# Kernel optimization log

Hardware: AMD Instinct MI355X
Metric: run time of the kernel (lower is better)

The kernel has to match this reference:

```python
import jax, jax.numpy as jnp
import numpy as np

B, H, S, D = 2, 8, 2048, 64

def setup_inputs() -> dict:
    key = jax.random.key(0)
    ks = jax.random.split(key, 6)
    names = ["Qx", "Kx", "Vx", "Qy", "Ky", "Vy"]
    return {n: jax.random.normal(k, (B, H, S, D), dtype=jnp.float32)
            for n, k in zip(names, ks)}

def reference(Qx, Kx, Vx, Qy, Ky, Vy):
    scale = float(np.sqrt(Qx.shape[-1]))
    # Two score matmuls: [B,H,S,S] each
    ax = jnp.einsum('bhqd,bhkd->bhqk', Qx, Kx)
    ay = jnp.einsum('bhqd,bhkd->bhqk', Qy, Ky)
    # cat(dim=1) -> reshape(B,2,H,S,S) -> mean(dim=1) == elementwise average
    attn = (ax + ay) * 0.5
    # numerically stable softmax over keys; dropout is identity in eval mode
    w = jax.nn.softmax(attn / scale, axis=-1)
    # Shared attention weights into two value matmuls
    out1 = jnp.einsum('bhqk,bhkd->bhqd', w, Vx)
    out2 = jnp.einsum('bhqk,bhkd->bhqd', w, Vy)
    return (out1, out2)
```

## Files before the change

kernel.cpp:

```cpp
#include <hip/hip_runtime.h>
#include <hip/hip_bf16.h>

typedef __attribute__((ext_vector_type(4)))  float f32x4;
typedef __attribute__((ext_vector_type(16))) float f32x16;
typedef __attribute__((ext_vector_type(8)))  short s16x8;
typedef __attribute__((ext_vector_type(4)))  short s16x4;
typedef __attribute__((ext_vector_type(4)))  int   i32x4;

#define BB 2
#define HH 8
#define SS 2048
#define DD 64
#define QBLK 64
#define KBLK 64
#define NT   (SS / KBLK)
#define NBH  (BB * HH)

#define WS_KX 0
#define WS_KY ((size_t)NBH * NT * 8192)
#define WS_VX ((size_t)2 * NBH * NT * 8192)
#define WS_VY ((size_t)3 * NBH * NT * 8192)
#define WS_NEED ((size_t)4 * NBH * NT * 8192)

__device__ __forceinline__ short f2bf(float x) {
    unsigned u = __builtin_bit_cast(unsigned, x);
    u = (u + 0x7FFFu + ((u >> 16) & 1u)) >> 16;
    return (short)u;
}

__device__ __forceinline__ unsigned cvtpk(float lo, float hi) {
    unsigned d;
    asm("v_cvt_pk_bf16_f32 %0, %1, %2" : "=v"(d) : "v"(lo), "v"(hi));
    return d;
}

__device__ __forceinline__ int swz(int row, int byteInRow) {
    return row * 128 + (byteInRow ^ ((row & 7) << 4));
}

__device__ __forceinline__ void glds16(const void* g, void* l) {
    __builtin_amdgcn_global_load_lds(
        (const __attribute__((address_space(1))) unsigned*)g,
        (__attribute__((address_space(3))) unsigned*)l, 16, 0, 0);
}

__global__ __launch_bounds__(256)
void prep_kv(const float* __restrict__ Kx, const float* __restrict__ Ky,
             const float* __restrict__ Vx, const float* __restrict__ Vy,
             char* __restrict__ ws)
{
    const int b = blockIdx.x;
    if (b < 1024) {
        const int tid  = b * 256 + threadIdx.x;
        const int dblk = tid & 7;
        const int s    = (tid >> 3) & 2047;
        const int bh   = tid >> 14;
        const size_t gi = ((size_t)bh * SS + s) * DD + dblk * 8;
        const int kt = s >> 6, row = s & 63;
        const size_t dst = (size_t)(bh * NT + kt) * 8192 + swz(row, dblk * 16);
        const float* px = Kx + gi;
        const float* py = Ky + gi;
        s16x8 a, bb;
#pragma unroll
        for (int i = 0; i < 8; ++i) { a[i] = f2bf(px[i]); bb[i] = f2bf(py[i]); }
        *(s16x8*)(ws + WS_KX + dst) = a;
        *(s16x8*)(ws + WS_KY + dst) = bb;
    } else {
        const int tid  = (b - 1024) * 256 + threadIdx.x;
        const int d    = tid & 63;
        const int sblk = (tid >> 6) & 7;
        const int kt   = (tid >> 9) & 31;
        const int bh   = tid >> 14;
        const size_t gbase = ((size_t)bh * SS + kt * 64 + sblk * 8) * DD + d;
        s16x8 a, bb;
#pragma unroll
        for (int i = 0; i < 8; ++i) {
            a[i]  = f2bf(Vx[gbase + (size_t)i * DD]);
            bb[i] = f2bf(Vy[gbase + (size_t)i * DD]);
        }
        const size_t dst = (size_t)(bh * NT + kt) * 8192 + swz(d, sblk * 16);
        *(s16x8*)(ws + WS_VX + dst) = a;
        *(s16x8*)(ws + WS_VY + dst) = bb;
    }
}

__global__ __launch_bounds__(256, 2)
void attn_main(const float* __restrict__ Qx, const float* __restrict__ Qy,
               const char* __restrict__ ws, float* __restrict__ Out)
{
    extern __shared__ char lds[];

    const int t    = threadIdx.x;
    const int lane = t & 63;
    const int w    = t >> 6;
    const int qsub = w & 1;
    const int ks   = w >> 1;
    const int l31  = lane & 31;
    const int hi   = lane >> 5;

    int bid = blockIdx.x;
    bid = (bid & 7) * 64 + (bid >> 3);
    const int bh = bid >> 5;
    const int q0 = (bid & 31) * QBLK;
    const size_t base = (size_t)bh * SS * DD;

    const int qrow = q0 + qsub * 32 + l31;
    s16x8 qbx[4], qby[4];
#pragma unroll
    for (int dc = 0; dc < 4; ++dc) {
        const int d0 = dc * 16 + hi * 8;
        const float* qp = Qx + base + (size_t)qrow * DD + d0;
        const float* qq = Qy + base + (size_t)qrow * DD + d0;
        const float4 f0 = *(const float4*)qp;
        const float4 f1 = *(const float4*)(qp + 4);
        const float4 h0 = *(const float4*)qq;
        const float4 h1 = *(const float4*)(qq + 4);
        qbx[dc][0]=f2bf(f0.x); qbx[dc][1]=f2bf(f0.y); qbx[dc][2]=f2bf(f0.z); qbx[dc][3]=f2bf(f0.w);
        qbx[dc][4]=f2bf(f1.x); qbx[dc][5]=f2bf(f1.y); qbx[dc][6]=f2bf(f1.z); qbx[dc][7]=f2bf(f1.w);
        qby[dc][0]=f2bf(h0.x); qby[dc][1]=f2bf(h0.y); qby[dc][2]=f2bf(h0.z); qby[dc][3]=f2bf(h0.w);
        qby[dc][4]=f2bf(h1.x); qby[dc][5]=f2bf(h1.y); qby[dc][6]=f2bf(h1.z); qby[dc][7]=f2bf(h1.w);
    }

    f32x16 o1_0, o1_1, o2_0, o2_1;
#pragma unroll
    for (int j = 0; j < 16; ++j) { o1_0[j] = 0.f; o1_1[j] = 0.f; o2_0[j] = 0.f; o2_1[j] = 0.f; }
    float lsum = 0.f;

    const float SCL = 0.09016844005556021f;

#define STAGE(kt_, b_)                                                             \
    do {                                                                           \
        const size_t img_ = (size_t)(bh * NT + (kt_)) * 8192 + (size_t)t * 16;     \
        char* dst_ = lds + (b_) * 32768 + t * 16;                                  \
        glds16(ws + WS_KX + img_,        dst_);                                    \
        glds16(ws + WS_KX + img_ + 4096, dst_ + 4096);                             \
        glds16(ws + WS_KY + img_,        dst_ + 8192);                             \
        glds16(ws + WS_KY + img_ + 4096, dst_ + 12288);                            \
        glds16(ws + WS_VX + img_,        dst_ + 16384);                            \
        glds16(ws + WS_VX + img_ + 4096, dst_ + 20480);                            \
        glds16(ws + WS_VY + img_,        dst_ + 24576);                            \
        glds16(ws + WS_VY + img_ + 4096, dst_ + 28672);                            \
    } while (0)

#define QK_BLOCK(KxL_, KyL_, sc_)                                                  \
    do {                                                                           \
        _Pragma("unroll")                                                          \
        for (int dc = 0; dc < 4; ++dc) {                                           \
            const int off = swz(ks * 32 + l31, dc * 32 + hi * 16);                 \
            const s16x8 ka = *(const s16x8*)((KxL_) + off);                        \
            const s16x8 kb = *(const s16x8*)((KyL_) + off);                        \
            sc_ = __builtin_amdgcn_mfma_f32_32x32x16_bf16(ka, qbx[dc], sc_, 0, 0, 0); \
            sc_ = __builtin_amdgcn_mfma_f32_32x32x16_bf16(kb, qby[dc], sc_, 0, 0, 0); \
        }                                                                          \
    } while (0)

#define V_READS(VxL_, VyL_, vr_)                                                   \
    do {                                                                           \
        _Pragma("unroll")                                                          \
        for (int ch = 0; ch < 2; ++ch) {                                           \
            const int off0 = swz(l31,      ks * 64 + ch * 32 + hi * 16);           \
            const int off1 = swz(32 + l31, ks * 64 + ch * 32 + hi * 16);           \
            vr_[ch * 4 + 0] = *(const s16x8*)((VxL_) + off0);                      \
            vr_[ch * 4 + 1] = *(const s16x8*)((VxL_) + off1);                      \
            vr_[ch * 4 + 2] = *(const s16x8*)((VyL_) + off0);                      \
            vr_[ch * 4 + 3] = *(const s16x8*)((VyL_) + off1);                      \
        }                                                                          \
    } while (0)

#define SOFTMAX_PA(sc_, pa_)                                                       \
    do {                                                                           \
        float s_ = 0.f;                                                            \
        _Pragma("unroll")                                                          \
        for (int j = 0; j < 16; ++j) { sc_[j] = exp2f(sc_[j] * SCL); s_ += sc_[j]; } \
        lsum += s_;                                                                \
        _Pragma("unroll")                                                          \
        for (int ch = 0; ch < 2; ++ch) {                                           \
            const int b8 = ch * 8;                                                 \
            unsigned x0 = cvtpk(sc_[b8 + 0], sc_[b8 + 1]);                         \
            unsigned x1 = cvtpk(sc_[b8 + 2], sc_[b8 + 3]);                         \
            unsigned y0 = cvtpk(sc_[b8 + 4], sc_[b8 + 5]);                         \
            unsigned y1 = cvtpk(sc_[b8 + 6], sc_[b8 + 7]);                         \
            asm("v_permlane32_swap_b32 %0, %1" : "+v"(x0), "+v"(y0));              \
            asm("v_permlane32_swap_b32 %0, %1" : "+v"(x1), "+v"(y1));              \
            i32x4 pw;                                                              \
            pw[0] = (int)x0; pw[1] = (int)x1; pw[2] = (int)y0; pw[3] = (int)y1;    \
            pa_[ch] = __builtin_bit_cast(s16x8, pw);                               \
        }                                                                          \
    } while (0)

#define PV_BLOCK(pa_, vr_)                                                         \
    do {                                                                           \
        _Pragma("unroll")                                                          \
        for (int ch = 0; ch < 2; ++ch) {                                           \
            o1_0 = __builtin_amdgcn_mfma_f32_32x32x16_bf16(pa_[ch], vr_[ch*4+0], o1_0, 0, 0, 0); \
            o1_1 = __builtin_amdgcn_mfma_f32_32x32x16_bf16(pa_[ch], vr_[ch*4+1], o1_1, 0, 0, 0); \
            o2_0 = __builtin_amdgcn_mfma_f32_32x32x16_bf16(pa_[ch], vr_[ch*4+2], o2_0, 0, 0, 0); \
            o2_1 = __builtin_amdgcn_mfma_f32_32x32x16_bf16(pa_[ch], vr_[ch*4+3], o2_1, 0, 0, 0); \
        }                                                                          \
    } while (0)

#define ZERO16(v_) { _Pragma("unroll") for (int j = 0; j < 16; ++j) (v_)[j] = 0.f; }

    STAGE(0, 0);
    __syncthreads();

    s16x8 pa[2];
    s16x8 vr[8];
    {
        const char* KxL = lds;
        const char* KyL = KxL + 8192;
        const char* VxL = KxL + 16384;
        const char* VyL = KxL + 24576;
        f32x16 sc;
        ZERO16(sc);
        __builtin_amdgcn_s_setprio(1);
        QK_BLOCK(KxL, KyL, sc);
        __builtin_amdgcn_s_setprio(0);
        V_READS(VxL, VyL, vr);
        SOFTMAX_PA(sc, pa);
    }
    STAGE(1, 1);
    __syncthreads();
    int cur = 1;

#pragma unroll 2
    for (int kt = 1; kt < NT; ++kt) {
        if (kt + 1 < NT) STAGE(kt + 1, cur ^ 1);

        const char* KxL = lds + cur * 32768;
        const char* KyL = KxL + 8192;
        const char* VxL = KxL + 16384;
        const char* VyL = KxL + 24576;

        f32x16 sc;
        ZERO16(sc);

        __builtin_amdgcn_s_setprio(1);
        QK_BLOCK(KxL, KyL, sc);

        s16x8 nvr[8];
        V_READS(VxL, VyL, nvr);

        PV_BLOCK(pa, vr);

        SOFTMAX_PA(sc, pa);
        __builtin_amdgcn_s_setprio(0);

#pragma unroll
        for (int i = 0; i < 8; ++i) vr[i] = nvr[i];

        __syncthreads();
        cur ^= 1;
    }

    __builtin_amdgcn_s_setprio(1);
    PV_BLOCK(pa, vr);
    __builtin_amdgcn_s_setprio(0);

#undef STAGE
#undef QK_BLOCK
#undef V_READS
#undef SOFTMAX_PA
#undef PV_BLOCK
#undef ZERO16

    const float lh = lsum + __shfl_xor(lsum, 32);

    __syncthreads();
    float* ex   = (float*)lds;
    float* linv = (float*)(lds + 24576);
    const int exo = (qsub * 64 + lane) * 33;
    float* O1 = Out;
    float* O2 = Out + (size_t)BB * HH * SS * DD;

    if (ks == 1) {
#pragma unroll
        for (int j = 0; j < 16; ++j) { ex[exo + j] = o1_0[j]; ex[exo + 16 + j] = o1_1[j]; }
        ex[exo + 32] = lh;
    }
    __syncthreads();
    if (ks == 0 && hi == 0)
        linv[qsub * 32 + l31] = 1.0f / (lh + ex[exo + 32]);
    __syncthreads();
    if (ks == 0) {
#pragma unroll
        for (int j = 0; j < 16; ++j) {
            const int qr = (j & 3) + 8 * (j >> 2) + 4 * hi;
            const float invj = linv[qsub * 32 + qr];
            const size_t ob = base + (size_t)(q0 + qsub * 32 + qr) * DD + l31;
            O1[ob]      = (o1_0[j] + ex[exo + j])      * invj;
            O1[ob + 32] = (o1_1[j] + ex[exo + 16 + j]) * invj;
        }
    }
    __syncthreads();
    if (ks == 1) {
#pragma unroll
        for (int j = 0; j < 16; ++j) { ex[exo + j] = o2_0[j]; ex[exo + 16 + j] = o2_1[j]; }
    }
    __syncthreads();
    if (ks == 0) {
#pragma unroll
        for (int j = 0; j < 16; ++j) {
            const int qr = (j & 3) + 8 * (j >> 2) + 4 * hi;
            const float invj = linv[qsub * 32 + qr];
            const size_t ob = base + (size_t)(q0 + qsub * 32 + qr) * DD + l31;
            O2[ob]      = (o2_0[j] + ex[exo + j])      * invj;
            O2[ob + 32] = (o2_1[j] + ex[exo + 16 + j]) * invj;
        }
    }
}

__global__ __launch_bounds__(256, 2)
void attn_dual_fallback(const float* __restrict__ Qx, const float* __restrict__ Kx,
                        const float* __restrict__ Vx, const float* __restrict__ Qy,
                        const float* __restrict__ Ky, const float* __restrict__ Vy,
                        float* __restrict__ Out)
{
    __shared__ __attribute__((aligned(16))) char lds[40960];
    char* KxL  = lds;
    char* KyL  = lds + 8192;
    char* VtxL = lds + 16384;
    char* VtyL = lds + 24576;

    const int t    = threadIdx.x;
    const int lane = t & 63;
    const int w    = t >> 6;
    const int g    = lane >> 4;
    const int c    = lane & 15;
    char* PL = lds + 32768 + w * 2048;

    const int bid = blockIdx.x;
    const int bh  = bid >> 5;
    const int q0  = (bid & 31) * 64;
    const size_t base = (size_t)bh * SS * DD;

    const int qrowA = q0 + w * 16 + c;
    s16x8 qxf[2], qyf[2];
#pragma unroll
    for (int kk = 0; kk < 2; ++kk) {
        const int d0 = kk * 32 + g * 8;
        const float* qp = Qx + base + (size_t)qrowA * DD + d0;
        const float* qq = Qy + base + (size_t)qrowA * DD + d0;
#pragma unroll
        for (int i = 0; i < 8; ++i) { qxf[kk][i] = f2bf(qp[i]); qyf[kk][i] = f2bf(qq[i]); }
    }

    f32x4 o1[4], o2[4];
#pragma unroll
    for (int n = 0; n < 4; ++n) {
        o1[n] = (f32x4){0.f, 0.f, 0.f, 0.f};
        o2[n] = (f32x4){0.f, 0.f, 0.f, 0.f};
    }
    float m[4]    = {-1e30f, -1e30f, -1e30f, -1e30f};
    float lsum[4] = {0.f, 0.f, 0.f, 0.f};
    const float SCL = 0.09016844005556021f;

    for (int kt = 0; kt < SS / 64; ++kt) {
        __syncthreads();
#pragma unroll
        for (int j = 0; j < 4; ++j) {
            const int f   = t + 256 * j;
            const int row = f >> 4;
            const int c4  = f & 15;
            const size_t gi = base + (size_t)(kt * 64 + row) * DD + c4 * 4;
            const float4 kx = *(const float4*)(Kx + gi);
            const float4 ky = *(const float4*)(Ky + gi);
            const float4 vx = *(const float4*)(Vx + gi);
            const float4 vy = *(const float4*)(Vy + gi);
            s16x4 a; a[0]=f2bf(kx.x); a[1]=f2bf(kx.y); a[2]=f2bf(kx.z); a[3]=f2bf(kx.w);
            *(s16x4*)(KxL + swz(row, c4 * 8)) = a;
            s16x4 b; b[0]=f2bf(ky.x); b[1]=f2bf(ky.y); b[2]=f2bf(ky.z); b[3]=f2bf(ky.w);
            *(s16x4*)(KyL + swz(row, c4 * 8)) = b;
            const int d0 = c4 * 4;
            *(short*)(VtxL + swz(d0 + 0, row * 2)) = f2bf(vx.x);
            *(short*)(VtxL + swz(d0 + 1, row * 2)) = f2bf(vx.y);
            *(short*)(VtxL + swz(d0 + 2, row * 2)) = f2bf(vx.z);
            *(short*)(VtxL + swz(d0 + 3, row * 2)) = f2bf(vx.w);
            *(short*)(VtyL + swz(d0 + 0, row * 2)) = f2bf(vy.x);
            *(short*)(VtyL + swz(d0 + 1, row * 2)) = f2bf(vy.y);
            *(short*)(VtyL + swz(d0 + 2, row * 2)) = f2bf(vy.z);
            *(short*)(VtyL + swz(d0 + 3, row * 2)) = f2bf(vy.w);
        }
        __syncthreads();

        f32x4 sc[4];
#pragma unroll
        for (int n = 0; n < 4; ++n) {
            f32x4 acc = (f32x4){0.f, 0.f, 0.f, 0.f};
            const int keyrow = n * 16 + c;
#pragma unroll
            for (int kk = 0; kk < 2; ++kk) {
                const int off = swz(keyrow, (kk * 32 + g * 8) * 2);
                const s16x8 kxf = *(const s16x8*)(KxL + off);
                const s16x8 kyf = *(const s16x8*)(KyL + off);
                acc = __builtin_amdgcn_mfma_f32_16x16x32_bf16(qxf[kk], kxf, acc, 0, 0, 0);
                acc = __builtin_amdgcn_mfma_f32_16x16x32_bf16(qyf[kk], kyf, acc, 0, 0, 0);
            }
            sc[n] = acc;
        }

#pragma unroll
        for (int r = 0; r < 4; ++r) {
            float v0 = fmaxf(fmaxf(sc[0][r], sc[1][r]), fmaxf(sc[2][r], sc[3][r])) * SCL;
#pragma unroll
            for (int off = 1; off < 16; off <<= 1) v0 = fmaxf(v0, __shfl_xor(v0, off));
            const float mnew = fmaxf(m[r], v0);
            const float cr = exp2f(m[r] - mnew);
            m[r] = mnew;
            float srow = 0.f;
#pragma unroll
            for (int n = 0; n < 4; ++n) {
                const float pp = exp2f(sc[n][r] * SCL - mnew);
                srow += pp;
                *(short*)(PL + swz(g * 4 + r, (n * 16 + c) * 2)) = f2bf(pp);
            }
#pragma unroll
            for (int off = 1; off < 16; off <<= 1) srow += __shfl_xor(srow, off);
            lsum[r] = lsum[r] * cr + srow;
#pragma unroll
            for (int n = 0; n < 4; ++n) { o1[n][r] *= cr; o2[n][r] *= cr; }
        }

        s16x8 pf[2];
#pragma unroll
        for (int kk = 0; kk < 2; ++kk)
            pf[kk] = *(const s16x8*)(PL + swz(c, (kk * 32 + g * 8) * 2));
#pragma unroll
        for (int nd = 0; nd < 4; ++nd) {
            const int drow = nd * 16 + c;
#pragma unroll
            for (int kk = 0; kk < 2; ++kk) {
                const int off = swz(drow, (kk * 32 + g * 8) * 2);
                const s16x8 vxf = *(const s16x8*)(VtxL + off);
                const s16x8 vyf = *(const s16x8*)(VtyL + off);
                o1[nd] = __builtin_amdgcn_mfma_f32_16x16x32_bf16(pf[kk], vxf, o1[nd], 0, 0, 0);
                o2[nd] = __builtin_amdgcn_mfma_f32_16x16x32_bf16(pf[kk], vyf, o2[nd], 0, 0, 0);
            }
        }
    }

    float* O1 = Out;
    float* O2 = Out + (size_t)BB * HH * SS * DD;
#pragma unroll
    for (int r = 0; r < 4; ++r) {
        const float inv = 1.0f / lsum[r];
        const int qrow = q0 + w * 16 + g * 4 + r;
        const size_t ob = base + (size_t)qrow * DD + c;
#pragma unroll
        for (int nd = 0; nd < 4; ++nd) {
            O1[ob + nd * 16] = o1[nd][r] * inv;
            O2[ob + nd * 16] = o2[nd][r] * inv;
        }
    }
}

extern "C" void kernel_launch(void* const* d_in, const int* in_sizes, int n_in,
                              void* d_out, int out_size, void* d_ws, size_t ws_size,
                              hipStream_t stream) {
    const float* Qx = (const float*)d_in[0];
    const float* Kx = (const float*)d_in[1];
    const float* Vx = (const float*)d_in[2];
    const float* Qy = (const float*)d_in[3];
    const float* Ky = (const float*)d_in[4];
    const float* Vy = (const float*)d_in[5];
    float* Out = (float*)d_out;

    if (ws_size >= WS_NEED) {
        char* ws = (char*)d_ws;
        hipLaunchKernelGGL(prep_kv, dim3(2048), dim3(256), 0, stream,
                           Kx, Ky, Vx, Vy, ws);
        hipFuncSetAttribute((const void*)attn_main,
                            hipFuncAttributeMaxDynamicSharedMemorySize, 65536);
        hipLaunchKernelGGL(attn_main, dim3(NBH * (SS / QBLK)), dim3(256), 65536,
                           stream, Qx, Qy, (const char*)ws, Out);
    } else {
        hipLaunchKernelGGL(attn_dual_fallback, dim3(NBH * 32), dim3(256),
                           0, stream, Qx, Kx, Vx, Qy, Ky, Vy, Out);
    }
}
```

Baseline: 63.20 us.

## Deepen software pipeline so softmax lags QK by one tile

Restructures the key-tile loop so each iteration computes QK scores for the next tile while running softmax and PV for the previous tile's scores, using two score accumulators alternated by a manual 2x unroll. The aim is to hide the QK MFMA latency behind the exp/softmax VALU work and PV MFMAs, instead of waiting on fresh scores each iteration. It also issues the second tile's global staging before the first QK. The cost is more live registers (two f32x16 score buffers plus V fragments), which may raise register pressure or lower occupancy, and the prologue and epilogue handling is more complex.

Result: no change. 63.03 us (-0.3%).

```diff
diff --git a/kernel.cpp b/kernel.cpp
--- a/kernel.cpp
+++ b/kernel.cpp
@@ -201,61 +201,62 @@
 
 #define ZERO16(v_) { _Pragma("unroll") for (int j = 0; j < 16; ++j) (v_)[j] = 0.f; }
 
-    STAGE(0, 0);
-    __syncthreads();
-
     s16x8 pa[2];
     s16x8 vr[8];
+    f32x16 scA, scB;
+
+    STAGE(0, 0);
+    __syncthreads();
+
     {
-        const char* KxL = lds;
-        const char* KyL = KxL + 8192;
-        const char* VxL = KxL + 16384;
-        const char* VyL = KxL + 24576;
-        f32x16 sc;
-        ZERO16(sc);
+        STAGE(1, 1);
+        ZERO16(scA);
         __builtin_amdgcn_s_setprio(1);
-        QK_BLOCK(KxL, KyL, sc);
+        QK_BLOCK(lds, lds + 8192, scA);
         __builtin_amdgcn_s_setprio(0);
-        V_READS(VxL, VyL, vr);
-        SOFTMAX_PA(sc, pa);
-    }
-    STAGE(1, 1);
-    __syncthreads();
-    int cur = 1;
-
-#pragma unroll 2
-    for (int kt = 1; kt < NT; ++kt) {
-        if (kt + 1 < NT) STAGE(kt + 1, cur ^ 1);
-
-        const char* KxL = lds + cur * 32768;
-        const char* KyL = KxL + 8192;
-        const char* VxL = KxL + 16384;
-        const char* VyL = KxL + 24576;
-
-        f32x16 sc;
-        ZERO16(sc);
-
+        V_READS(lds + 16384, lds + 24576, vr);
+    }
+    __syncthreads();
+
+#define ITER(kt_, bufc_, scN_, scP_)                                               \
+    do {                                                                           \
+        if ((kt_) + 1 < NT) STAGE((kt_) + 1, (bufc_) ^ 1);                         \
+        const char* KxL_ = lds + (bufc_) * 32768;                                  \
+        const char* KyL_ = KxL_ + 8192;                                            \
+        const char* VxL_ = KxL_ + 16384;                                           \
+        const char* VyL_ = KxL_ + 24576;                                           \
+        ZERO16(scN_);                                                              \
+        s16x8 nvr_[8];                                                             \
+        __builtin_amdgcn_s_setprio(1);                                             \
+        QK_BLOCK(KxL_, KyL_, scN_);                                                \
+        V_READS(VxL_, VyL_, nvr_);                                                 \
+        SOFTMAX_PA(scP_, pa);                                                      \
+        PV_BLOCK(pa, vr);                                                          \
+        __builtin_amdgcn_s_setprio(0);                                             \
+        _Pragma("unroll")                                                          \
+        for (int i_ = 0; i_ < 8; ++i_) vr[i_] = nvr_[i_];                          \
+        __syncthreads();                                                           \
+    } while (0)
+
+    for (int kt = 1; kt + 1 < NT; kt += 2) {
+        ITER(kt,     1, scB, scA);
+        ITER(kt + 1, 0, scA, scB);
+    }
+
+    {
+        const char* KxL_ = lds + 32768;
+        ZERO16(scB);
         __builtin_amdgcn_s_setprio(1);
-        QK_BLOCK(KxL, KyL, sc);
-
-        s16x8 nvr[8];
-        V_READS(VxL, VyL, nvr);
-
+        QK_BLOCK(KxL_, KxL_ + 8192, scB);
+        SOFTMAX_PA(scA, pa);
         PV_BLOCK(pa, vr);
-
-        SOFTMAX_PA(sc, pa);
         __builtin_amdgcn_s_setprio(0);
-
-#pragma unroll
-        for (int i = 0; i < 8; ++i) vr[i] = nvr[i];
-
-        __syncthreads();
-        cur ^= 1;
-    }
-
-    __builtin_amdgcn_s_setprio(1);
-    PV_BLOCK(pa, vr);
-    __builtin_amdgcn_s_setprio(0);
+        V_READS(KxL_ + 16384, KxL_ + 24576, vr);
+        __builtin_amdgcn_s_setprio(1);
+        SOFTMAX_PA(scB, pa);
+        PV_BLOCK(pa, vr);
+        __builtin_amdgcn_s_setprio(0);
+    }
 
 #undef STAGE
 #undef QK_BLOCK
@@ -263,6 +264,7 @@
 #undef SOFTMAX_PA
 #undef PV_BLOCK
 #undef ZERO16
+#undef ITER
 
     const float lh = lsum + __shfl_xor(lsum, 32);
 
```

## Enlarge query tile to 128 with 512-thread blocks and 128-key stages

Applied to the files above, without the earlier changes.

Doubles the query block to 128 rows using 8 waves (4 query sub-tiles × 2 key splits). Each pipeline stage now loads two 64-key tiles (128 KB LDS double-buffered), so K/V traffic per query row halves. The loop processes both key halves per iteration and drops the previous software pipelining that overlapped the PV product of one tile with the QK product of the next. The cost is fewer blocks (256 total), heavy LDS use that likely allows only one block per CU despite the launch bounds of 2, and less overlap inside each wave.

Result: faster. 59.46 us (median of 2 runs) (-5.9%).

```diff
diff --git a/kernel.cpp b/kernel.cpp
--- a/kernel.cpp
+++ b/kernel.cpp
@@ -11,9 +11,9 @@
 #define HH 8
 #define SS 2048
 #define DD 64
-#define QBLK 64
-#define KBLK 64
-#define NT   (SS / KBLK)
+#define QBLK 128
+#define NT   32
+#define NT2  16
 #define NBH  (BB * HH)
 
 #define WS_KX 0
@@ -84,7 +84,7 @@
     }
 }
 
-__global__ __launch_bounds__(256, 2)
+__global__ __launch_bounds__(512, 2)
 void attn_main(const float* __restrict__ Qx, const float* __restrict__ Qy,
                const char* __restrict__ ws, float* __restrict__ Out)
 {
@@ -93,15 +93,15 @@
     const int t    = threadIdx.x;
     const int lane = t & 63;
     const int w    = t >> 6;
-    const int qsub = w & 1;
-    const int ks   = w >> 1;
+    const int qsub = w & 3;
+    const int ks   = w >> 2;
     const int l31  = lane & 31;
     const int hi   = lane >> 5;
 
     int bid = blockIdx.x;
-    bid = (bid & 7) * 64 + (bid >> 3);
-    const int bh = bid >> 5;
-    const int q0 = (bid & 31) * QBLK;
+    bid = (bid & 7) * 32 + (bid >> 3);
+    const int bh = bid >> 4;
+    const int q0 = (bid & 15) * QBLK;
     const size_t base = (size_t)bh * SS * DD;
 
     const int qrow = q0 + qsub * 32 + l31;
@@ -130,40 +130,44 @@
 
 #define STAGE(kt_, b_)                                                             \
     do {                                                                           \
-        const size_t img_ = (size_t)(bh * NT + (kt_)) * 8192 + (size_t)t * 16;     \
-        char* dst_ = lds + (b_) * 32768 + t * 16;                                  \
+        const size_t img_ = (size_t)(bh * NT + (kt_) * 2) * 8192 + (size_t)t * 16; \
+        char* dst_ = lds + (b_) * 65536 + t * 16;                                  \
         glds16(ws + WS_KX + img_,        dst_);                                    \
-        glds16(ws + WS_KX + img_ + 4096, dst_ + 4096);                             \
-        glds16(ws + WS_KY + img_,        dst_ + 8192);                             \
-        glds16(ws + WS_KY + img_ + 4096, dst_ + 12288);                            \
-        glds16(ws + WS_VX + img_,        dst_ + 16384);                            \
-        glds16(ws + WS_VX + img_ + 4096, dst_ + 20480);                            \
-        glds16(ws + WS_VY + img_,        dst_ + 24576);                            \
-        glds16(ws + WS_VY + img_ + 4096, dst_ + 28672);                            \
+        glds16(ws + WS_KX + img_ + 8192, dst_ + 8192);                             \
+        glds16(ws + WS_KY + img_,        dst_ + 16384);                            \
+        glds16(ws + WS_KY + img_ + 8192, dst_ + 24576);                            \
+        glds16(ws + WS_VX + img_,        dst_ + 32768);                            \
+        glds16(ws + WS_VX + img_ + 8192, dst_ + 40960);                            \
+        glds16(ws + WS_VY + img_,        dst_ + 49152);                            \
+        glds16(ws + WS_VY + img_ + 8192, dst_ + 57344);                            \
     } while (0)
 
-#define QK_BLOCK(KxL_, KyL_, sc_)                                                  \
+#define QK_BLOCK(buf_, h_, sc_)                                                    \
     do {                                                                           \
+        const char* KxI_ = (buf_) + ks * 8192;                                     \
+        const char* KyI_ = (buf_) + 16384 + ks * 8192;                             \
         _Pragma("unroll")                                                          \
         for (int dc = 0; dc < 4; ++dc) {                                           \
-            const int off = swz(ks * 32 + l31, dc * 32 + hi * 16);                 \
-            const s16x8 ka = *(const s16x8*)((KxL_) + off);                        \
-            const s16x8 kb = *(const s16x8*)((KyL_) + off);                        \
+            const int off = swz((h_) * 32 + l31, dc * 32 + hi * 16);               \
+            const s16x8 ka = *(const s16x8*)(KxI_ + off);                          \
+            const s16x8 kb = *(const s16x8*)(KyI_ + off);                          \
             sc_ = __builtin_amdgcn_mfma_f32_32x32x16_bf16(ka, qbx[dc], sc_, 0, 0, 0); \
             sc_ = __builtin_amdgcn_mfma_f32_32x32x16_bf16(kb, qby[dc], sc_, 0, 0, 0); \
         }                                                                          \
     } while (0)
 
-#define V_READS(VxL_, VyL_, vr_)                                                   \
+#define V_READS(buf_, h_, vr_)                                                     \
     do {                                                                           \
+        const char* VxI_ = (buf_) + 32768 + ks * 8192;                             \
+        const char* VyI_ = (buf_) + 49152 + ks * 8192;                             \
         _Pragma("unroll")                                                          \
         for (int ch = 0; ch < 2; ++ch) {                                           \
-            const int off0 = swz(l31,      ks * 64 + ch * 32 + hi * 16);           \
-            const int off1 = swz(32 + l31, ks * 64 + ch * 32 + hi * 16);           \
-            vr_[ch * 4 + 0] = *(const s16x8*)((VxL_) + off0);                      \
-            vr_[ch * 4 + 1] = *(const s16x8*)((VxL_) + off1);                      \
-            vr_[ch * 4 + 2] = *(const s16x8*)((VyL_) + off0);                      \
-            vr_[ch * 4 + 3] = *(const s16x8*)((VyL_) + off1);                      \
+            const int off0 = swz(l31,      (h_) * 64 + ch * 32 + hi * 16);         \
+            const int off1 = swz(32 + l31, (h_) * 64 + ch * 32 + hi * 16);         \
+            vr_[ch * 4 + 0] = *(const s16x8*)(VxI_ + off0);                        \
+            vr_[ch * 4 + 1] = *(const s16x8*)(VxI_ + off1);                        \
+            vr_[ch * 4 + 2] = *(const s16x8*)(VyI_ + off0);                        \
+            vr_[ch * 4 + 3] = *(const s16x8*)(VyI_ + off1);                        \
         }                                                                          \
     } while (0)
 
@@ -203,59 +207,30 @@
 
     STAGE(0, 0);
     __syncthreads();
-
-    s16x8 pa[2];
-    s16x8 vr[8];
-    {
-        const char* KxL = lds;
-        const char* KyL = KxL + 8192;
-        const char* VxL = KxL + 16384;
-        const char* VyL = KxL + 24576;
-        f32x16 sc;
-        ZERO16(sc);
+    int cur = 0;
+
+    for (int kt = 0; kt < NT2; ++kt) {
+        if (kt + 1 < NT2) STAGE(kt + 1, cur ^ 1);
+
+        const char* buf = lds + cur * 65536;
+        f32x16 scA, scB;
+        ZERO16(scA); ZERO16(scB);
+        s16x8 pa[2], vrA[8], vrB[8];
+
         __builtin_amdgcn_s_setprio(1);
-        QK_BLOCK(KxL, KyL, sc);
+        QK_BLOCK(buf, 0, scA);
+        QK_BLOCK(buf, 1, scB);
+        V_READS(buf, 0, vrA);
+        SOFTMAX_PA(scA, pa);
+        PV_BLOCK(pa, vrA);
+        V_READS(buf, 1, vrB);
+        SOFTMAX_PA(scB, pa);
+        PV_BLOCK(pa, vrB);
         __builtin_amdgcn_s_setprio(0);
-        V_READS(VxL, VyL, vr);
-        SOFTMAX_PA(sc, pa);
-    }
-    STAGE(1, 1);
-    __syncthreads();
-    int cur = 1;
-
-#pragma unroll 2
-    for (int kt = 1; kt < NT; ++kt) {
-        if (kt + 1 < NT) STAGE(kt + 1, cur ^ 1);
-
-        const char* KxL = lds + cur * 32768;
-        const char* KyL = KxL + 8192;
-        const char* VxL = KxL + 16384;
-        const char* VyL = KxL + 24576;
-
-        f32x16 sc;
-        ZERO16(sc);
-
-        __builtin_amdgcn_s_setprio(1);
-        QK_BLOCK(KxL, KyL, sc);
-
-        s16x8 nvr[8];
-        V_READS(VxL, VyL, nvr);
-
-        PV_BLOCK(pa, vr);
-
-        SOFTMAX_PA(sc, pa);
-        __builtin_amdgcn_s_setprio(0);
-
-#pragma unroll
-        for (int i = 0; i < 8; ++i) vr[i] = nvr[i];
 
         __syncthreads();
         cur ^= 1;
     }
-
-    __builtin_amdgcn_s_setprio(1);
-    PV_BLOCK(pa, vr);
-    __builtin_amdgcn_s_setprio(0);
 
 #undef STAGE
 #undef QK_BLOCK
@@ -268,7 +243,7 @@
 
     __syncthreads();
     float* ex   = (float*)lds;
-    float* linv = (float*)(lds + 24576);
+    float* linv = (float*)(lds + 65536);
     const int exo = (qsub * 64 + lane) * 33;
     float* O1 = Out;
     float* O2 = Out + (size_t)BB * HH * SS * DD;
@@ -470,8 +445,8 @@
         hipLaunchKernelGGL(prep_kv, dim3(2048), dim3(256), 0, stream,
                            Kx, Ky, Vx, Vy, ws);
         hipFuncSetAttribute((const void*)attn_main,
-                            hipFuncAttributeMaxDynamicSharedMemorySize, 65536);
-        hipLaunchKernelGGL(attn_main, dim3(NBH * (SS / QBLK)), dim3(256), 65536,
+                            hipFuncAttributeMaxDynamicSharedMemorySize, 131072);
+        hipLaunchKernelGGL(attn_main, dim3(NBH * (SS / QBLK)), dim3(512), 131072,
                            stream, Qx, Qy, (const char*)ws, Out);
     } else {
         hipLaunchKernelGGL(attn_dual_fallback, dim3(NBH * 32), dim3(256),
```
